# Optimization experiments

Hardware: AMD Instinct MI355X
Metric: run time of the kernel (lower is better)

## Reference

```python
import jax, jax.numpy as jnp
import numpy as np

EPS = 1e-12  # matches torch F.normalize default eps

def l2norm(t):
    n = jnp.linalg.norm(t, axis=-1, keepdims=True)
    return t / jnp.maximum(n, EPS)

def rotate_half(x):
    # '... (j d) -> ... j d' with j=2: split into two halves, return cat(-x2, x1)
    x1, x2 = jnp.split(x, 2, axis=-1)
    return jnp.concatenate((-x2, x1), axis=-1)

def rotary_freqs(seq_len, dim):
    inv_freq = 1.0 / (10000.0 ** (jnp.arange(0, dim, 2, dtype=jnp.float32) / dim))
    seq = jnp.arange(seq_len, dtype=jnp.float32)
    freqs = seq[:, None] * inv_freq[None, :]          # [n, d/2]
    emb = jnp.concatenate((freqs, freqs), axis=-1)    # [n, d]
    return emb[None, None]                            # [1, 1, n, d]

def apply_rotary_pos_emb(t, freqs):
    # rot_dim == dim_head here, so the pass-through slice is empty
    return t * jnp.cos(freqs) + rotate_half(t) * jnp.sin(freqs)

def setup_inputs() -> dict:
    key = jax.random.key(0)
    kq, kk, kv = jax.random.split(key, 3)
    b, h, n, d = 2, 16, 2048, 64
    q = jax.random.normal(kq, (b, h, n, d), dtype=jnp.float32)
    k = jax.random.normal(kk, (b, h, n, d), dtype=jnp.float32)
    v = jax.random.normal(kv, (b, h, n, d), dtype=jnp.float32)
    q_scale = jnp.ones((d,), dtype=jnp.float32)
    k_scale = jnp.ones((d,), dtype=jnp.float32)
    return {"q": q, "k": k, "v": v, "q_scale": q_scale, "k_scale": k_scale}

def reference(q, k, v, q_scale, k_scale):
    b, h, n, d = q.shape
    # QK RMSNorm (l2 normalize + learned per-dim scale)
    q = l2norm(q) * q_scale
    k = l2norm(k) * k_scale
    # rotary position embedding (always applied in the source module)
    freqs = rotary_freqs(n, d)
    q = apply_rotary_pos_emb(q, freqs)
    k = apply_rotary_pos_emb(k, freqs)
    # attention: explicit scores -> softmax -> values
    scale = d ** -0.5
    sim = jnp.einsum('bhid,bhjd->bhij', q, k) * scale
    attn = jax.nn.softmax(sim, axis=-1)
    out = jnp.einsum('bhij,bhjd->bhid', attn, v)
    # 'b h n d -> b n (h d)'
    return out.transpose(0, 2, 1, 3).reshape(b, n, h * d)
```

## Files before the change

### kernel.cpp

```cpp
#include <hip/hip_runtime.h>
#include <math.h>

#define BH   32
#define NSEQ 2048
#define DH   64
#define NH   16
#define LOG2E 1.44269504088896f

typedef _Float16 f16x8 __attribute__((ext_vector_type(8)));
typedef __fp16   fp16x2 __attribute__((ext_vector_type(2)));
typedef _Float16 half2v __attribute__((ext_vector_type(2)));
typedef float    f32x16v __attribute__((ext_vector_type(16)));
typedef unsigned uint2v __attribute__((ext_vector_type(2)));

#if __has_builtin(__builtin_amdgcn_exp2f)
#define EXP2F(x) __builtin_amdgcn_exp2f(x)
#else
#define EXP2F(x) exp2f(x)
#endif

static __device__ __forceinline__ unsigned pkrtz(float a, float b) {
    fp16x2 r = __builtin_amdgcn_cvt_pkrtz(a, b);
    return __builtin_bit_cast(unsigned, r);
}
static __device__ __forceinline__ unsigned packh_rne(float a, float b) {
    union { _Float16 h[2]; unsigned u; } x;
    x.h[0] = (_Float16)a; x.h[1] = (_Float16)b;
    return x.u;
}

static __device__ __forceinline__ float2 rope_cs(int pos, int p) {
    float invf_rev = EXP2F(-(float)p * (13.287712379549449f / 32.0f)) * 0.15915494309189535f;
    float rev = (float)pos * invf_rev;
    float fr = rev - floorf(rev);
    float th = fr * 6.283185307179586f;
    return make_float2(__cosf(th), __sinf(th));
}

__global__ __launch_bounds__(256) void prep_all(
    const float* __restrict__ q, const float* __restrict__ k, const float* __restrict__ v,
    const float* __restrict__ qs, const float* __restrict__ ksc,
    unsigned* __restrict__ qh, unsigned* __restrict__ kh, unsigned* __restrict__ vt2) {
    const int bid = blockIdx.x;
    const int t = threadIdx.x;
    if (bid < 16384) {
        const bool isq = bid < 8192;
        const float* in = isq ? q : k;
        const float* sc = isq ? qs : ksc;
        const float smul = isq ? 0.125f * LOG2E : 1.0f;
        const int sb = bid & 8191;
        const int w = t >> 6, lane = t & 63;
        const int c = lane & 31, hfr = lane >> 5;
        const int row = sb * 8 + w * 2 + hfr;
        float2 x2 = *(const float2*)(in + (size_t)row * DH + 2 * c);
        float ss = x2.x * x2.x + x2.y * x2.y;
        #pragma unroll
        for (int off = 16; off > 0; off >>= 1) ss += __shfl_xor(ss, off);
        float inv = 1.0f / fmaxf(sqrtf(ss), 1e-12f);
        float2 s2 = *(const float2*)(sc + 2 * c);
        float t0 = x2.x * inv * s2.x;
        float t1 = x2.y * inv * s2.y;
        float p0 = __shfl_xor(t0, 16);
        float p1 = __shfl_xor(t1, 16);
        float r0 = (c < 16) ? -p0 : p0;
        float r1 = (c < 16) ? -p1 : p1;
        int pos = row & (NSEQ - 1);
        int pp = (2 * c) & 31;
        float2 cs0 = rope_cs(pos, pp);
        float2 cs1 = rope_cs(pos, pp + 1);
        float o0 = (t0 * cs0.x + r0 * cs0.y) * smul;
        float o1 = (t1 * cs1.x + r1 * cs1.y) * smul;
        unsigned val = packh_rne(o0, o1);
        if (isq) {
            qh[row * 32 + c] = val;
        } else {
            const int rloc = row & (NSEQ - 1);
            const unsigned idx = (unsigned)((rloc >> 5) * 1024 + (c >> 3) * 256
                               + ((c >> 2) & 1) * 128 + (rloc & 31) * 4 + (c & 3));
            kh[(size_t)(row >> 11) * 65536 + idx] = val;
        }
    } else {
        const int sb = bid - 16384;
        const int kt = sb & 31, bh = sb >> 5;
        __shared__ float Lv[64 * 68];
        #pragma unroll
        for (int i = 0; i < 4; ++i) {
            int chunk = t + 256 * i;
            int r = chunk >> 4, fg = chunk & 15;
            *(float4*)&Lv[r * 68 + fg * 4] =
                *(const float4*)(v + ((size_t)bh * NSEQ + kt * 64 + r) * DH + fg * 4);
        }
        __syncthreads();
        const int d = t & 63, kg = t >> 6;
        unsigned u[8];
        #pragma unroll
        for (int j = 0; j < 8; ++j) {
            int ky = kg * 16 + 2 * j;
            u[j] = pkrtz(Lv[ky * 68 + d], Lv[(ky + 1) * 68 + d]);
        }
        const int rh = d >> 5, cc = d & 31;
        unsigned* dst = vt2 + (size_t)bh * 65536
                      + (size_t)((kt * 4 + kg) * 2 + rh) * 256 + cc * 4;
        *(uint4*)(dst)       = make_uint4(u[0], u[1], u[2], u[3]);
        *(uint4*)(dst + 128) = make_uint4(u[4], u[5], u[6], u[7]);
    }
}

static __device__ __forceinline__ f16x8 ld8(const unsigned* p) {
    return *(const f16x8*)p;
}

static __device__ __forceinline__ void pv_tile(
    f32x16v& s, const f16x8 (&vc)[4], f32x16v (&ot)[2], float& lp, int hf)
{
    #pragma unroll
    for (int r = 0; r < 16; ++r) s[r] = EXP2F(s[r]);
    #pragma unroll
    for (int kk = 0; kk < 2; ++kk) {
        unsigned P01 = pkrtz(s[kk * 8 + 0], s[kk * 8 + 1]);
        unsigned P23 = pkrtz(s[kk * 8 + 2], s[kk * 8 + 3]);
        unsigned P45 = pkrtz(s[kk * 8 + 4], s[kk * 8 + 5]);
        unsigned P67 = pkrtz(s[kk * 8 + 6], s[kk * 8 + 7]);
#if __has_builtin(__builtin_amdgcn_fdot2)
        const half2v one2 = {(_Float16)1.0f, (_Float16)1.0f};
        lp = __builtin_amdgcn_fdot2(__builtin_bit_cast(half2v, P01), one2, lp, false);
        lp = __builtin_amdgcn_fdot2(__builtin_bit_cast(half2v, P23), one2, lp, false);
        lp = __builtin_amdgcn_fdot2(__builtin_bit_cast(half2v, P45), one2, lp, false);
        lp = __builtin_amdgcn_fdot2(__builtin_bit_cast(half2v, P67), one2, lp, false);
#else
        #pragma unroll
        for (int r = 0; r < 8; ++r) lp += s[kk * 8 + r];
#endif
        union { unsigned u[4]; f16x8 v; } B;
#if __has_builtin(__builtin_amdgcn_permlane32_swap)
        uint2v r02 = __builtin_amdgcn_permlane32_swap(P01, P45, 0, 0);
        uint2v r13 = __builtin_amdgcn_permlane32_swap(P23, P67, 0, 0);
        B.u[0] = r02[0]; B.u[1] = r13[0]; B.u[2] = r02[1]; B.u[3] = r13[1];
#else
        unsigned x01 = (unsigned)__shfl_xor((int)P01, 32);
        unsigned x23 = (unsigned)__shfl_xor((int)P23, 32);
        unsigned x45 = (unsigned)__shfl_xor((int)P45, 32);
        unsigned x67 = (unsigned)__shfl_xor((int)P67, 32);
        B.u[0] = hf ? x45 : P01;
        B.u[1] = hf ? x67 : P23;
        B.u[2] = hf ? P45 : x01;
        B.u[3] = hf ? P67 : x23;
#endif
        ot[0] = __builtin_amdgcn_mfma_f32_32x32x16_f16(vc[kk * 2 + 0], B.v, ot[0], 0, 0, 0);
        ot[1] = __builtin_amdgcn_mfma_f32_32x32x16_f16(vc[kk * 2 + 1], B.v, ot[1], 0, 0, 0);
    }
}

static __device__ __forceinline__ void attn_step(
    const f16x8 (&kc)[4], const f16x8 (&vc)[4],
    f16x8 (&kn)[4], f16x8 (&vn)[4],
    const unsigned* kp, const unsigned* vp, bool pre,
    const f16x8 (&qf)[2][4], f32x16v (&o)[2][2], float (&lp)[2],
    const f32x16v& z16, int hf)
{
    if (pre) {
        #pragma unroll
        for (int ks = 0; ks < 4; ++ks) kn[ks] = ld8(kp + ks * 256);
        #pragma unroll
        for (int kk = 0; kk < 2; ++kk)
            #pragma unroll
            for (int rh = 0; rh < 2; ++rh)
                vn[kk * 2 + rh] = ld8(vp + kk * 512 + rh * 256);
    }
    f32x16v s0 = __builtin_amdgcn_mfma_f32_32x32x16_f16(kc[0], qf[0][0], z16, 0, 0, 0);
    f32x16v s1 = __builtin_amdgcn_mfma_f32_32x32x16_f16(kc[0], qf[1][0], z16, 0, 0, 0);
    #pragma unroll
    for (int ks = 1; ks < 4; ++ks) {
        s0 = __builtin_amdgcn_mfma_f32_32x32x16_f16(kc[ks], qf[0][ks], s0, 0, 0, 0);
        s1 = __builtin_amdgcn_mfma_f32_32x32x16_f16(kc[ks], qf[1][ks], s1, 0, 0, 0);
    }
    pv_tile(s0, vc, o[0], lp[0], hf);
    pv_tile(s1, vc, o[1], lp[1], hf);
}

__global__ __launch_bounds__(256, 2) void attn_kernel(
    const unsigned* __restrict__ qh, const unsigned* __restrict__ kf,
    const unsigned* __restrict__ vf, float* __restrict__ out) {

    __shared__ float Lred[128 * 33];

    const int flat = (blockIdx.x & 7) * 64 + (blockIdx.x >> 3);
    const int bh = flat >> 4, qb = flat & 15;

    const int tid = threadIdx.x;
    const int w = tid >> 6, lane = tid & 63;
    const int c = lane & 31, hf = lane >> 5;
    const int qhw = w & 1;
    const int khw = w >> 1;

    const _Float16* qbase = (const _Float16*)qh + ((size_t)bh * NSEQ + qb * 128) * DH;
    f16x8 qf[2][4];
    #pragma unroll
    for (int t = 0; t < 2; ++t)
        #pragma unroll
        for (int ks = 0; ks < 4; ++ks)
            qf[t][ks] = *(const f16x8*)(qbase + (t * 64 + qhw * 32 + c) * DH + ks * 16 + hf * 8);

    const unsigned* kfb = kf + (size_t)bh * 65536 + khw * 1024 + lane * 4;
    const unsigned* vfb = vf + (size_t)bh * 65536 + khw * 1024 + lane * 4;

    f16x8 ka[4], va[4], kb[4], vb[4];
    #pragma unroll
    for (int ks = 0; ks < 4; ++ks) ka[ks] = ld8(kfb + ks * 256);
    #pragma unroll
    for (int kk = 0; kk < 2; ++kk)
        #pragma unroll
        for (int rh = 0; rh < 2; ++rh)
            va[kk * 2 + rh] = ld8(vfb + kk * 512 + rh * 256);

    f32x16v z16;
    #pragma unroll
    for (int r = 0; r < 16; ++r) z16[r] = 0.f;

    f32x16v o[2][2];
    #pragma unroll
    for (int t = 0; t < 2; ++t)
        #pragma unroll
        for (int mt = 0; mt < 2; ++mt)
            #pragma unroll
            for (int r = 0; r < 16; ++r) o[t][mt][r] = 0.f;
    float lp[2] = {0.f, 0.f};

    for (int jt = 0; jt < 32; jt += 2) {
        attn_step(ka, va, kb, vb,
                  kfb + (size_t)(jt + 1) * 2048, vfb + (size_t)(jt + 1) * 2048,
                  true, qf, o, lp, z16, hf);
        attn_step(kb, vb, ka, va,
                  kfb + (size_t)(jt + 2) * 2048, vfb + (size_t)(jt + 2) * 2048,
                  jt + 2 < 32, qf, o, lp, z16, hf);
    }

    float lw[2];
    #pragma unroll
    for (int t = 0; t < 2; ++t) lw[t] = lp[t] + __shfl_xor(lp[t], 32);

    const int b = bh >> 4, h = bh & 15;
    #pragma unroll
    for (int t = 0; t < 2; ++t) {
        if (t) __syncthreads();
        if (w >= 2) {
            const int base = ((w - 2) * 64 + lane) * 33;
            #pragma unroll
            for (int mt = 0; mt < 2; ++mt)
                #pragma unroll
                for (int r = 0; r < 16; ++r) Lred[base + mt * 16 + r] = o[t][mt][r];
            Lred[base + 32] = lw[t];
        }
        __syncthreads();
        if (w < 2) {
            const int base = (w * 64 + lane) * 33;
            #pragma unroll
            for (int mt = 0; mt < 2; ++mt)
                #pragma unroll
                for (int r = 0; r < 16; ++r) o[t][mt][r] += Lred[base + mt * 16 + r];
            float invl = 1.0f / (lw[t] + Lred[base + 32]);
            const int pos = qb * 128 + t * 64 + w * 32 + c;
            float* obase = out + ((size_t)b * NSEQ + pos) * (NH * DH) + h * DH;
            #pragma unroll
            for (int mt = 0; mt < 2; ++mt)
                #pragma unroll
                for (int g = 0; g < 4; ++g) {
                    float4 r4 = make_float4(o[t][mt][g * 4 + 0] * invl, o[t][mt][g * 4 + 1] * invl,
                                            o[t][mt][g * 4 + 2] * invl, o[t][mt][g * 4 + 3] * invl);
                    *(float4*)(obase + mt * 32 + g * 8 + hf * 4) = r4;
                }
        }
    }
}

extern "C" void kernel_launch(void* const* d_in, const int* in_sizes, int n_in,
                              void* d_out, int out_size, void* d_ws, size_t ws_size,
                              hipStream_t stream) {
    const float* q  = (const float*)d_in[0];
    const float* k  = (const float*)d_in[1];
    const float* v  = (const float*)d_in[2];
    const float* qs = (const float*)d_in[3];
    const float* ks = (const float*)d_in[4];
    float* outp = (float*)d_out;

    unsigned* qh  = (unsigned*)d_ws;
    unsigned* kh  = qh + (size_t)BH * NSEQ * 32;
    unsigned* vt2 = kh + (size_t)BH * NSEQ * 32;

    prep_all<<<17408, 256, 0, stream>>>(q, k, v, qs, ks, qh, kh, vt2);
    attn_kernel<<<512, 256, 0, stream>>>(qh, kh, vt2, outp);
}
```

Before: 143.6 us.

## Software-pipeline QK of next tile with softmax/PV of current tile

Restructures the main attention loop so that the QK^T MFMAs for the next key tile are issued before the exp/pack/PV work of the current tile, which lets the matrix core overlap with the VALU softmax work. K and V register buffers are reduced from double sets to single sets, with loads placed just after their last use. MFMA sections are wrapped in s_setprio to favour matrix issue across waves. This keeps two score tiles live at once, which raises register pressure under launch_bounds(256,2). Loads also get less lead time before use, so global-load latency may be exposed.

```diff
diff --git a/kernel.cpp b/kernel.cpp
--- a/kernel.cpp
+++ b/kernel.cpp
@@ -110,6 +110,33 @@
     return *(const f16x8*)p;
 }
 
+static __device__ __forceinline__ void load_k(f16x8 (&kd)[4], const unsigned* p) {
+    #pragma unroll
+    for (int ks = 0; ks < 4; ++ks) kd[ks] = ld8(p + ks * 256);
+}
+static __device__ __forceinline__ void load_v(f16x8 (&vd)[4], const unsigned* p) {
+    #pragma unroll
+    for (int kk = 0; kk < 2; ++kk)
+        #pragma unroll
+        for (int rh = 0; rh < 2; ++rh)
+            vd[kk * 2 + rh] = ld8(p + kk * 512 + rh * 256);
+}
+
+static __device__ __forceinline__ void qk2(
+    const f16x8 (&kc)[4], const f16x8 (&qf)[2][4], const f32x16v& z16,
+    f32x16v& s0, f32x16v& s1)
+{
+    __builtin_amdgcn_s_setprio(1);
+    s0 = __builtin_amdgcn_mfma_f32_32x32x16_f16(kc[0], qf[0][0], z16, 0, 0, 0);
+    s1 = __builtin_amdgcn_mfma_f32_32x32x16_f16(kc[0], qf[1][0], z16, 0, 0, 0);
+    #pragma unroll
+    for (int ks = 1; ks < 4; ++ks) {
+        s0 = __builtin_amdgcn_mfma_f32_32x32x16_f16(kc[ks], qf[0][ks], s0, 0, 0, 0);
+        s1 = __builtin_amdgcn_mfma_f32_32x32x16_f16(kc[ks], qf[1][ks], s1, 0, 0, 0);
+    }
+    __builtin_amdgcn_s_setprio(0);
+}
+
 static __device__ __forceinline__ void pv_tile(
     f32x16v& s, const f16x8 (&vc)[4], f32x16v (&ot)[2], float& lp, int hf)
 {
@@ -146,34 +173,17 @@
         B.u[2] = hf ? P45 : x01;
         B.u[3] = hf ? P67 : x23;
 #endif
+        __builtin_amdgcn_s_setprio(1);
         ot[0] = __builtin_amdgcn_mfma_f32_32x32x16_f16(vc[kk * 2 + 0], B.v, ot[0], 0, 0, 0);
         ot[1] = __builtin_amdgcn_mfma_f32_32x32x16_f16(vc[kk * 2 + 1], B.v, ot[1], 0, 0, 0);
-    }
-}
-
-static __device__ __forceinline__ void attn_step(
-    const f16x8 (&kc)[4], const f16x8 (&vc)[4],
-    f16x8 (&kn)[4], f16x8 (&vn)[4],
-    const unsigned* kp, const unsigned* vp, bool pre,
-    const f16x8 (&qf)[2][4], f32x16v (&o)[2][2], float (&lp)[2],
-    const f32x16v& z16, int hf)
+        __builtin_amdgcn_s_setprio(0);
+    }
+}
+
+static __device__ __forceinline__ void smpv2(
+    f32x16v& s0, f32x16v& s1, const f16x8 (&vc)[4],
+    f32x16v (&o)[2][2], float (&lp)[2], int hf)
 {
-    if (pre) {
-        #pragma unroll
-        for (int ks = 0; ks < 4; ++ks) kn[ks] = ld8(kp + ks * 256);
-        #pragma unroll
-        for (int kk = 0; kk < 2; ++kk)
-            #pragma unroll
-            for (int rh = 0; rh < 2; ++rh)
-                vn[kk * 2 + rh] = ld8(vp + kk * 512 + rh * 256);
-    }
-    f32x16v s0 = __builtin_amdgcn_mfma_f32_32x32x16_f16(kc[0], qf[0][0], z16, 0, 0, 0);
-    f32x16v s1 = __builtin_amdgcn_mfma_f32_32x32x16_f16(kc[0], qf[1][0], z16, 0, 0, 0);
-    #pragma unroll
-    for (int ks = 1; ks < 4; ++ks) {
-        s0 = __builtin_amdgcn_mfma_f32_32x32x16_f16(kc[ks], qf[0][ks], s0, 0, 0, 0);
-        s1 = __builtin_amdgcn_mfma_f32_32x32x16_f16(kc[ks], qf[1][ks], s1, 0, 0, 0);
-    }
     pv_tile(s0, vc, o[0], lp[0], hf);
     pv_tile(s1, vc, o[1], lp[1], hf);
 }
@@ -204,15 +214,6 @@
     const unsigned* kfb = kf + (size_t)bh * 65536 + khw * 1024 + lane * 4;
     const unsigned* vfb = vf + (size_t)bh * 65536 + khw * 1024 + lane * 4;
 
-    f16x8 ka[4], va[4], kb[4], vb[4];
-    #pragma unroll
-    for (int ks = 0; ks < 4; ++ks) ka[ks] = ld8(kfb + ks * 256);
-    #pragma unroll
-    for (int kk = 0; kk < 2; ++kk)
-        #pragma unroll
-        for (int rh = 0; rh < 2; ++rh)
-            va[kk * 2 + rh] = ld8(vfb + kk * 512 + rh * 256);
-
     f32x16v z16;
     #pragma unroll
     for (int r = 0; r < 16; ++r) z16[r] = 0.f;
@@ -226,13 +227,26 @@
             for (int r = 0; r < 16; ++r) o[t][mt][r] = 0.f;
     float lp[2] = {0.f, 0.f};
 
+    f16x8 kc[4], vc[4];
+    f32x16v sA0, sA1, sB0, sB1;
+
+    load_k(kc, kfb);
+    load_v(vc, vfb);
+    qk2(kc, qf, z16, sA0, sA1);
+    load_k(kc, kfb + 2048);
+
     for (int jt = 0; jt < 32; jt += 2) {
-        attn_step(ka, va, kb, vb,
-                  kfb + (size_t)(jt + 1) * 2048, vfb + (size_t)(jt + 1) * 2048,
-                  true, qf, o, lp, z16, hf);
-        attn_step(kb, vb, ka, va,
-                  kfb + (size_t)(jt + 2) * 2048, vfb + (size_t)(jt + 2) * 2048,
-                  jt + 2 < 32, qf, o, lp, z16, hf);
+        qk2(kc, qf, z16, sB0, sB1);
+        if (jt + 2 < 32) load_k(kc, kfb + (size_t)(jt + 2) * 2048);
+        smpv2(sA0, sA1, vc, o, lp, hf);
+        load_v(vc, vfb + (size_t)(jt + 1) * 2048);
+
+        if (jt + 2 < 32) {
+            qk2(kc, qf, z16, sA0, sA1);
+            if (jt + 3 < 32) load_k(kc, kfb + (size_t)(jt + 3) * 2048);
+        }
+        smpv2(sB0, sB1, vc, o, lp, hf);
+        if (jt + 2 < 32) load_v(vc, vfb + (size_t)(jt + 2) * 2048);
     }
 
     float lw[2];
@@ -245,19 +259,21 @@
         if (t) __syncthreads();
         if (w >= 2) {
             const int base = ((w - 2) * 64 + lane) * 33;
+            f32x16v* ov = (t == 0) ? &o[0][0] : &o[1][0];
             #pragma unroll
             for (int mt = 0; mt < 2; ++mt)
                 #pragma unroll
-                for (int r = 0; r < 16; ++r) Lred[base + mt * 16 + r] = o[t][mt][r];
+                for (int r = 0; r < 16; ++r) Lred[base + mt * 16 + r] = ov[mt][r];
             Lred[base + 32] = lw[t];
         }
         __syncthreads();
         if (w < 2) {
             const int base = (w * 64 + lane) * 33;
+            f32x16v* ov = (t == 0) ? &o[0][0] : &o[1][0];
             #pragma unroll
             for (int mt = 0; mt < 2; ++mt)
                 #pragma unroll
-                for (int r = 0; r < 16; ++r) o[t][mt][r] += Lred[base + mt * 16 + r];
+                for (int r = 0; r < 16; ++r) ov[mt][r] += Lred[base + mt * 16 + r];
             float invl = 1.0f / (lw[t] + Lred[base + 32]);
             const int pos = qb * 128 + t * 64 + w * 32 + c;
             float* obase = out + ((size_t)b * NSEQ + pos) * (NH * DH) + h * DH;
@@ -265,8 +281,8 @@
             for (int mt = 0; mt < 2; ++mt)
                 #pragma unroll
                 for (int g = 0; g < 4; ++g) {
-                    float4 r4 = make_float4(o[t][mt][g * 4 + 0] * invl, o[t][mt][g * 4 + 1] * invl,
-                                            o[t][mt][g * 4 + 2] * invl, o[t][mt][g * 4 + 3] * invl);
+                    float4 r4 = make_float4(ov[mt][g * 4 + 0] * invl, ov[mt][g * 4 + 1] * invl,
+                                            ov[mt][g * 4 + 2] * invl, ov[mt][g * 4 + 3] * invl);
                     *(float4*)(obase + mt * 32 + g * 8 + hf * 4) = r4;
                 }
         }
```

New measurement: 140.8 us. No clear change (-1.9%).
